# Kernel optimization log

Hardware: AMD Instinct MI355X
Metric: run time of the kernel (lower is better)

## Reference

```python
import jax, jax.numpy as jnp
import numpy as np

B = 4          # documents per batch
L = 128        # unique candidate entity links
S = 2048       # predicted spans (max over batch)
N = 1 + L + S  # root + links + spans


def setup_inputs() -> dict:
    key = jax.random.key(0)
    k1, k2, k3 = jax.random.split(key, 3)
    # coref/linking edge scores over [root | links | spans] x [root | links | spans]
    scores = jax.random.normal(k1, (B, N, N), dtype=jnp.float32) * 0.1
    eye = jnp.eye(N, dtype=jnp.float32)
    # z mask: all admissible edges -- no self loops, no incoming edges to root
    z_mask = jnp.ones((B, N, N), dtype=jnp.float32) * (1.0 - eye)[None]
    z_mask = z_mask.at[:, :, 0].set(0.0)
    # target mask: sparse subset of z edges + root->all so a spanning
    # arborescence always exists (mirrors the gold cluster / gold link edges)
    tgt = (jax.random.uniform(k2, (B, N, N)) < 0.05).astype(jnp.float32) * z_mask
    tgt = tgt.at[:, 0, 1:].set(1.0)
    # ragged valid lengths per batch element (1 + unique_links_len + n_pred_spans)
    lengths = jnp.array([N, N - 256, N - 512, N - 64], dtype=jnp.int32)
    return {"scores": scores, "target_mask": tgt, "z_mask": z_mask, "lengths": lengths}


def _mtt_log_partition(scores, mask, lengths):
    """Matrix-tree theorem log-partition: logdet of the root-minor of the
    Laplacian of exp(scores) restricted to edges in `mask` and to the first
    `lengths[b]` nodes of each batch element."""
    n = scores.shape[-1]
    valid = (jnp.arange(n)[None, :] < lengths[:, None]).astype(scores.dtype)  # [B,N]
    w = jnp.exp(scores) * mask * valid[:, :, None] * valid[:, None, :]        # [B,N,N]
    colsum = jnp.sum(w, axis=-2)                                              # incoming weight per node
    lap = colsum[:, :, None] * jnp.eye(n, dtype=scores.dtype)[None] - w       # L = D_in - W
    minor = lap[:, 1:, 1:]                                                    # drop root row/col
    # pad the diagonal of invalid (past-length) nodes with 1 so they
    # contribute logdet 0 instead of making the minor singular
    pad = 1.0 - valid[:, 1:]
    minor = minor + pad[:, :, None] * jnp.eye(n - 1, dtype=scores.dtype)[None]
    _, logdet = jnp.linalg.slogdet(minor)
    return logdet


def reference(scores, target_mask, z_mask, lengths):
    log_z = _mtt_log_partition(scores, z_mask, lengths)        # log partition over all arborescences
    log_t = _mtt_log_partition(scores, target_mask, lengths)   # log weight of gold arborescences
    return jnp.mean(log_z - log_t)                             # MTT negative log-likelihood
```

## Files before the change

### kernel.cpp

```cpp
#include <hip/hip_runtime.h>
#include <math.h>

#define NFULL 2177
#define NN    2176
#define NB    64
#define NMAT  8
#define NBATCH 4
#define TP    65
#define LTP   132
#define UTP   188
#define QL    (16 * LTP)
#define QU    (16 * UTP)
#define QBUF  (QL + QU)
#define SSZ2  (2 * QBUF)


__global__ void init_cs_kernel(float* __restrict__ cs) {
  int i = blockIdx.x * blockDim.x + threadIdx.x;
  if (i < NMAT * NN) cs[i] = 0.f;
}

__global__ __launch_bounds__(256) void build_fused(const float* __restrict__ scores,
                                                   const float* __restrict__ zm,
                                                   const float* __restrict__ tm,
                                                   const int* __restrict__ lengths,
                                                   float* __restrict__ cs,
                                                   float* __restrict__ M) {
  int c = blockIdx.x * 256 + threadIdx.x;
  if (c >= NN) return;
  int b = blockIdx.z;
  int len = lengths[b];
  int j = c + 1;
  bool jv = (j < len);
  int r0 = blockIdx.y * 64;
  size_t sbase = (size_t)b * NFULL * NFULL + j;
  float az = 0.f, at = 0.f;
  if (blockIdx.y == 0 && jv) {
    float e = __expf(scores[sbase]);
    az += e * zm[sbase];
    at += e * tm[sbase];
  }
  size_t mz = (size_t)b * NN * NN + (size_t)r0 * NN + c;
  size_t mt = (size_t)(NBATCH + b) * NN * NN + (size_t)r0 * NN + c;
  for (int rr = 0; rr < 64; ++rr) {
    int i = r0 + rr + 1;
    float vz = 0.f, vt = 0.f;
    if (jv && i < len) {
      size_t off = sbase + (size_t)i * NFULL;
      float e = __expf(scores[off]);
      vz = e * zm[off];
      vt = e * tm[off];
      az += vz;
      at += vt;
    }
    M[mz] = -vz;
    M[mt] = -vt;
    mz += NN;
    mt += NN;
  }
  if (az != 0.f) atomicAdd(&cs[b * NN + c], az);
  if (at != 0.f) atomicAdd(&cs[(NBATCH + b) * NN + c], at);
}

__global__ void diag_fix(const int* __restrict__ lengths,
                         const float* __restrict__ cs,
                         float* __restrict__ M) {
  int idx = blockIdx.x * 256 + threadIdx.x;
  if (idx >= NMAT * NN) return;
  int mm = idx / NN, c = idx - mm * NN;
  int len = lengths[mm & 3];
  float pad = (c + 1 < len) ? 0.f : 1.f;
  M[(size_t)mm * NN * NN + (size_t)c * NN + c] = cs[idx] + pad;
}


__device__ __forceinline__ void factor64(float* T, int tid) {
  int c = tid & 63, g = tid >> 6;
  for (int j = 0; j < 63; ++j) {
    float inv = 1.0f / T[j * TP + j];
    int rs = j + 1 + ((g - j - 1) & 3);
    if (c == j) {
      for (int r = rs; r < 64; r += 4) T[r * TP + j] *= inv;
    }
    __syncthreads();
    if (c > j) {
      float ujc = T[j * TP + c];
      for (int r = rs; r < 64; r += 4) T[r * TP + c] -= T[r * TP + j] * ujc;
    }
    __syncthreads();
  }
}

__device__ void invert64(const float* T, float* X,
                         float* __restrict__ invUg,
                         float* __restrict__ invLg, int tid) {
  if (tid < 64) {
    int o = (tid >> 5) * 32, jj = tid & 31, j = o + jj;
    X[(o + jj) * TP + j] = 1.0f / T[(o + jj) * TP + (o + jj)];
    for (int i = jj - 1; i >= 0; --i) {
      float s = 0.f;
      for (int t = i + 1; t <= jj; ++t)
        s += T[(o + i) * TP + (o + t)] * X[(o + t) * TP + j];
      X[(o + i) * TP + j] = -s / T[(o + i) * TP + (o + i)];
    }
  }
  __syncthreads();
  for (int e = tid; e < 1024; e += 256) {
    int i = e >> 5, j = e & 31;
    float s = 0.f;
    for (int t = 0; t <= j; ++t)
      s += T[i * TP + 32 + t] * X[(32 + t) * TP + 32 + j];
    X[(32 + i) * TP + j] = s;
  }
  __syncthreads();
  for (int e = tid; e < 1024; e += 256) {
    int i = e >> 5, j = e & 31;
    float s = 0.f;
    for (int t = i; t < 32; ++t)
      s += X[i * TP + t] * X[(32 + t) * TP + j];
    X[i * TP + 32 + j] = -s;
  }
  __syncthreads();
  for (int e = tid; e < 4096; e += 256) {
    int i = e >> 6, j = e & 63;
    float v = 0.f;
    if (i < 32 && j >= 32) v = X[i * TP + j];
    else if ((i >> 5) == (j >> 5) && i <= j) v = X[i * TP + j];
    invUg[e] = v;
  }
  __syncthreads();
  if (tid < 64) {
    int o = (tid >> 5) * 32, jj = tid & 31, j = o + jj;
    X[(o + jj) * TP + j] = 1.0f;
    for (int i = jj + 1; i < 32; ++i) {
      float s = 0.f;
      for (int t = jj; t < i; ++t)
        s += T[(o + i) * TP + (o + t)] * X[(o + t) * TP + j];
      X[(o + i) * TP + j] = -s;
    }
  }
  __syncthreads();
  for (int e = tid; e < 1024; e += 256) {
    int i = e >> 5, j = e & 31;
    float s = 0.f;
    for (int t = j; t < 32; ++t)
      s += T[(32 + i) * TP + t] * X[t * TP + j];
    X[i * TP + 32 + j] = s;
  }
  __syncthreads();
  for (int e = tid; e < 1024; e += 256) {
    int i = e >> 5, j = e & 31;
    float s = 0.f;
    for (int t = 0; t <= i; ++t)
      s += X[(32 + i) * TP + 32 + t] * X[t * TP + 32 + j];
    X[(32 + i) * TP + j] = -s;
  }
  __syncthreads();
  for (int e = tid; e < 4096; e += 256) {
    int i = e >> 6, j = e & 63;
    float v = 0.f;
    if (i >= 32 && j < 32) v = X[i * TP + j];
    else if ((i >> 5) == (j >> 5)) v = (i > j) ? X[i * TP + j] : (i == j ? 1.f : 0.f);
    invLg[e] = v;
  }
}

__global__ __launch_bounds__(256) void factor0(float* __restrict__ Mb,
                                               float* __restrict__ invUb,
                                               float* __restrict__ invLb) {
  __shared__ float T[64 * TP];
  __shared__ float X[64 * TP];
  int m = blockIdx.x, tid = threadIdx.x;
  float* A = Mb + (size_t)m * NN * NN;
  for (int idx = tid; idx < 4096; idx += 256)
    T[(idx >> 6) * TP + (idx & 63)] = A[(size_t)(idx >> 6) * NN + (idx & 63)];
  __syncthreads();
  factor64(T, tid);
  for (int idx = tid; idx < 4096; idx += 256)
    A[(size_t)(idx >> 6) * NN + (idx & 63)] = T[(idx >> 6) * TP + (idx & 63)];
  invert64(T, X, invUb + (size_t)m * 4096, invLb + (size_t)m * 4096, tid);
}

__global__ __launch_bounds__(256) void panel_gemm(float* __restrict__ Mb,
                                                  const float* __restrict__ invUb,
                                                  const float* __restrict__ invLb,
                                                  int k0) {
  __shared__ float Aa[64][68];
  __shared__ float Bb[64][68];
  int m = blockIdx.y, role = blockIdx.z, tid = threadIdx.x;
  float* A = Mb + (size_t)m * NN * NN;
  int obase = k0 + 64 + blockIdx.x * 64;
  if (role == 0) {
    const float* invU = invUb + (size_t)m * 4096;
    for (int idx = tid; idx < 4096; idx += 256) {
      int r = idx >> 6, k = idx & 63;
      Aa[k][r] = A[(size_t)(obase + r) * NN + (k0 + k)];
    }
    for (int idx = tid; idx < 4096; idx += 256)
      Bb[idx >> 6][idx & 63] = invU[idx];
  } else {
    const float* invL = invLb + (size_t)m * 4096;
    for (int idx = tid; idx < 4096; idx += 256) {
      int r = idx >> 6, k = idx & 63;
      Aa[k][r] = invL[(r << 6) + k];
    }
    for (int idx = tid; idx < 4096; idx += 256) {
      int k = idx >> 6, c = idx & 63;
      Bb[k][c] = A[(size_t)(k0 + k) * NN + (obase + c)];
    }
  }
  __syncthreads();
  int c0 = (tid & 15) << 2;
  int r0 = (tid >> 4) << 2;
  float acc[4][4];
#pragma unroll
  for (int i = 0; i < 4; ++i)
#pragma unroll
    for (int jj = 0; jj < 4; ++jj) acc[i][jj] = 0.f;
#pragma unroll 8
  for (int k = 0; k < 64; ++k) {
    float4 a  = *(const float4*)&Aa[k][r0];
    float4 bv = *(const float4*)&Bb[k][c0];
    acc[0][0] += a.x * bv.x; acc[0][1] += a.x * bv.y; acc[0][2] += a.x * bv.z; acc[0][3] += a.x * bv.w;
    acc[1][0] += a.y * bv.x; acc[1][1] += a.y * bv.y; acc[1][2] += a.y * bv.z; acc[1][3] += a.y * bv.w;
    acc[2][0] += a.z * bv.x; acc[2][1] += a.z * bv.y; acc[2][2] += a.z * bv.z; acc[2][3] += a.z * bv.w;
    acc[3][0] += a.w * bv.x; acc[3][1] += a.w * bv.y; acc[3][2] += a.w * bv.z; acc[3][3] += a.w * bv.w;
  }
  if (role == 0) {
#pragma unroll
    for (int i = 0; i < 4; ++i) {
      float4 v = make_float4(acc[i][0], acc[i][1], acc[i][2], acc[i][3]);
      *(float4*)&A[(size_t)(obase + r0 + i) * NN + (k0 + c0)] = v;
    }
  } else {
#pragma unroll
    for (int i = 0; i < 4; ++i) {
      float4 v = make_float4(acc[i][0], acc[i][1], acc[i][2], acc[i][3]);
      *(float4*)&A[(size_t)(k0 + r0 + i) * NN + (obase + c0)] = v;
    }
  }
}


__device__ __forceinline__ void load_quarter_regs(const float* __restrict__ A,
                                                  int rbase, int cbase, int rows, int cols,
                                                  int kb, float* lr, float* ur, int tid) {
#pragma unroll
  for (int s = 0; s < 8; ++s) {
    int idx = tid + s * 256;
    int k = idx & 15, r = idx >> 4;
    int gr = rbase + (r < rows ? r : 0);
    lr[s] = A[(size_t)gr * NN + kb + k];
  }
#pragma unroll
  for (int s = 0; s < 8; ++s) {
    int idx = tid + s * 256;
    int c = idx & 127, k = idx >> 7;
    int gc = cbase + (c < cols ? c : 0);
    ur[s] = A[(size_t)(kb + k) * NN + gc];
  }
}

__device__ __forceinline__ void write_quarter_lds(float* __restrict__ S,
                                                  const float* lr, const float* ur, int tid) {
#pragma unroll
  for (int s = 0; s < 8; ++s) {
    int idx = tid + s * 256;
    int k = idx & 15, r = idx >> 4;
    S[k * LTP + r] = lr[s];
  }
#pragma unroll
  for (int s = 0; s < 8; ++s) {
    int idx = tid + s * 256;
    int c = idx & 127, k = idx >> 7;
    S[QL + k * UTP + c + 4 * (c >> 3)] = ur[s];
  }
}

__global__ __launch_bounds__(256, 2) void trail_gemm(float* __restrict__ Mb,
                                                     float* __restrict__ invUb,
                                                     float* __restrict__ invLb,
                                                     int k0, int do_inv) {
  __shared__ float S[SSZ2];
  int m = blockIdx.x;
  int txt = blockIdx.y, tyt = blockIdx.z;
  float* A = Mb + (size_t)m * NN * NN;
  int base = k0 + NB;
  int rem  = NN - base;
  int rbase = base + tyt * 128, cbase = base + txt * 128;
  int rows = rem - tyt * 128; if (rows > 128) rows = 128;
  int cols = rem - txt * 128; if (cols > 128) cols = 128;
  int tid = threadIdx.x;
  int tx = tid & 15, ty = tid >> 4;
  int rr = ty * 8, cc = tx * 8;
  int ccs = 12 * tx;
  float acc[8][8];
#pragma unroll
  for (int i = 0; i < 8; ++i)
#pragma unroll
    for (int j = 0; j < 8; ++j) acc[i][j] = 0.f;

  float lr[8], ur[8];
  load_quarter_regs(A, rbase, cbase, rows, cols, k0, lr, ur, tid);
  write_quarter_lds(S, lr, ur, tid);
  __syncthreads();

#pragma unroll
  for (int q = 0; q < 4; ++q) {
    if (q < 3)
      load_quarter_regs(A, rbase, cbase, rows, cols, k0 + (q + 1) * 16, lr, ur, tid);
    const float* Sc = S + (q & 1) * QBUF;
#pragma unroll
    for (int k = 0; k < 16; ++k) {
      const float* lp = &Sc[k * LTP + rr];
      const float* up = &Sc[QL + k * UTP + ccs];
      float4 a0 = *(const float4*)lp;
      float4 a1 = *(const float4*)(lp + 4);
      float4 b0 = *(const float4*)up;
      float4 b1 = *(const float4*)(up + 4);
      acc[0][0] += a0.x * b0.x; acc[0][1] += a0.x * b0.y; acc[0][2] += a0.x * b0.z; acc[0][3] += a0.x * b0.w;
      acc[0][4] += a0.x * b1.x; acc[0][5] += a0.x * b1.y; acc[0][6] += a0.x * b1.z; acc[0][7] += a0.x * b1.w;
      acc[1][0] += a0.y * b0.x; acc[1][1] += a0.y * b0.y; acc[1][2] += a0.y * b0.z; acc[1][3] += a0.y * b0.w;
      acc[1][4] += a0.y * b1.x; acc[1][5] += a0.y * b1.y; acc[1][6] += a0.y * b1.z; acc[1][7] += a0.y * b1.w;
      acc[2][0] += a0.z * b0.x; acc[2][1] += a0.z * b0.y; acc[2][2] += a0.z * b0.z; acc[2][3] += a0.z * b0.w;
      acc[2][4] += a0.z * b1.x; acc[2][5] += a0.z * b1.y; acc[2][6] += a0.z * b1.z; acc[2][7] += a0.z * b1.w;
      acc[3][0] += a0.w * b0.x; acc[3][1] += a0.w * b0.y; acc[3][2] += a0.w * b0.z; acc[3][3] += a0.w * b0.w;
      acc[3][4] += a0.w * b1.x; acc[3][5] += a0.w * b1.y; acc[3][6] += a0.w * b1.z; acc[3][7] += a0.w * b1.w;
      acc[4][0] += a1.x * b0.x; acc[4][1] += a1.x * b0.y; acc[4][2] += a1.x * b0.z; acc[4][3] += a1.x * b0.w;
      acc[4][4] += a1.x * b1.x; acc[4][5] += a1.x * b1.y; acc[4][6] += a1.x * b1.z; acc[4][7] += a1.x * b1.w;
      acc[5][0] += a1.y * b0.x; acc[5][1] += a1.y * b0.y; acc[5][2] += a1.y * b0.z; acc[5][3] += a1.y * b0.w;
      acc[5][4] += a1.y * b1.x; acc[5][5] += a1.y * b1.y; acc[5][6] += a1.y * b1.z; acc[5][7] += a1.y * b1.w;
      acc[6][0] += a1.z * b0.x; acc[6][1] += a1.z * b0.y; acc[6][2] += a1.z * b0.z; acc[6][3] += a1.z * b0.w;
      acc[6][4] += a1.z * b1.x; acc[6][5] += a1.z * b1.y; acc[6][6] += a1.z * b1.z; acc[6][7] += a1.z * b1.w;
      acc[7][0] += a1.w * b0.x; acc[7][1] += a1.w * b0.y; acc[7][2] += a1.w * b0.z; acc[7][3] += a1.w * b0.w;
      acc[7][4] += a1.w * b1.x; acc[7][5] += a1.w * b1.y; acc[7][6] += a1.w * b1.z; acc[7][7] += a1.w * b1.w;
    }
    __syncthreads();
    if (q < 3) {
      write_quarter_lds(S + ((q + 1) & 1) * QBUF, lr, ur, tid);
      __syncthreads();
    }
  }

  bool special = (txt == 0 && tyt == 0);
  if (!special) {
    if (cc < cols) {
#pragma unroll
      for (int i = 0; i < 8; ++i) {
        int r = rr + i;
        if (r < rows) {
          float4* p = (float4*)&A[(size_t)(rbase + r) * NN + cbase + cc];
          float4 v0 = p[0], v1 = p[1];
          v0.x -= acc[i][0]; v0.y -= acc[i][1]; v0.z -= acc[i][2]; v0.w -= acc[i][3];
          v1.x -= acc[i][4]; v1.y -= acc[i][5]; v1.z -= acc[i][6]; v1.w -= acc[i][7];
          p[0] = v0; p[1] = v1;
        }
      }
    }
    return;
  }
  float* T = S;
  float* X = S + 4224;
  if (cc < cols) {
#pragma unroll
    for (int i = 0; i < 8; ++i) {
      int r = rr + i;
      if (r < rows) {
        float4* p = (float4*)&A[(size_t)(rbase + r) * NN + cbase + cc];
        float4 v0 = p[0], v1 = p[1];
        v0.x -= acc[i][0]; v0.y -= acc[i][1]; v0.z -= acc[i][2]; v0.w -= acc[i][3];
        v1.x -= acc[i][4]; v1.y -= acc[i][5]; v1.z -= acc[i][6]; v1.w -= acc[i][7];
        if (r < 64 && cc < 64) {
          float* t = &T[r * TP + cc];
          t[0] = v0.x; t[1] = v0.y; t[2] = v0.z; t[3] = v0.w;
          t[4] = v1.x; t[5] = v1.y; t[6] = v1.z; t[7] = v1.w;
        } else {
          p[0] = v0; p[1] = v1;
        }
      }
    }
  }
  __syncthreads();
  factor64(T, tid);
  for (int idx = tid; idx < 4096; idx += 256) {
    int r = idx >> 6, c = idx & 63;
    A[(size_t)(base + r) * NN + base + c] = T[r * TP + c];
  }
  if (do_inv)
    invert64(T, X, invUb + (size_t)m * 4096, invLb + (size_t)m * 4096, tid);
}


__global__ void logdet_kernel(const float* __restrict__ Mb, double* __restrict__ dlog) {
  int m = blockIdx.x;
  const float* A = Mb + (size_t)m * NN * NN;
  double s = 0.0;
  for (int i = threadIdx.x; i < NN; i += 256)
    s += (double)logf(fabsf(A[(size_t)i * NN + i]));
  __shared__ double red[256];
  red[threadIdx.x] = s;
  __syncthreads();
  for (int k = 128; k > 0; k >>= 1) {
    if (threadIdx.x < k) red[threadIdx.x] += red[threadIdx.x + k];
    __syncthreads();
  }
  if (threadIdx.x == 0) dlog[m] = red[0];
}

__global__ void final_kernel(const double* __restrict__ dlog, float* __restrict__ out) {
  if (threadIdx.x == 0) {
    double acc = 0.0;
    for (int b = 0; b < NBATCH; ++b) acc += dlog[b] - dlog[NBATCH + b];
    out[0] = (float)(acc * 0.25);
  }
}


extern "C" void kernel_launch(void* const* d_in, const int* in_sizes, int n_in,
                              void* d_out, int out_size, void* d_ws, size_t ws_size,
                              hipStream_t stream) {
  const float* scores  = (const float*)d_in[0];
  const float* tm      = (const float*)d_in[1];
  const float* zm      = (const float*)d_in[2];
  const int*   lengths = (const int*)d_in[3];
  float* out = (float*)d_out;

  float* M  = (float*)d_ws;
  float* cs = M + (size_t)NMAT * NN * NN;
  double* dlog = (double*)(cs + (size_t)NMAT * NN);
  float* invU = (float*)(dlog + NMAT);
  float* invL = invU + (size_t)NMAT * 4096;

  init_cs_kernel<<<(NMAT * NN + 255) / 256, 256, 0, stream>>>(cs);
  build_fused<<<dim3((NN + 255) / 256, NN / 64, NBATCH), 256, 0, stream>>>(
      scores, zm, tm, lengths, cs, M);
  diag_fix<<<(NMAT * NN + 255) / 256, 256, 0, stream>>>(lengths, cs, M);
  factor0<<<NMAT, 256, 0, stream>>>(M, invU, invL);

  for (int k0 = 0; k0 + NB < NN; k0 += NB) {
    int rem = NN - k0 - NB;
    panel_gemm<<<dim3(rem / 64, NMAT, 2), 256, 0, stream>>>(M, invU, invL, k0);
    int nt = (rem + 127) / 128;
    trail_gemm<<<dim3(NMAT, nt, nt), 256, 0, stream>>>(
        M, invU, invL, k0, rem > 64 ? 1 : 0);
  }

  logdet_kernel<<<NMAT, 256, 0, stream>>>(M, dlog);
  final_kernel<<<1, 64, 0, stream>>>(dlog, out);
}
```

Before: 4.872 ms.

## Fuse LU pipeline into one persistent cooperative kernel with per-matrix ragged bounds

Replaces the per-step panel/trailing kernel launches (about 68 iterations of two launches each) and the setup kernels with a single cooperative persistent kernel that uses grid-wide syncs between phases. Work per step is also trimmed per matrix to the valid length rounded up to 64, so padded identity rows and columns of shorter documents are no longer factored. This removes launch overhead and wasted tiles. In exchange it adds grid.sync costs, runtime job-index decoding, and relies on the occupancy query to size the grid correctly.

```diff
diff --git a/kernel.cpp b/kernel.cpp
--- a/kernel.cpp
+++ b/kernel.cpp
@@ -1,5 +1,8 @@
 #include <hip/hip_runtime.h>
+#include <hip/hip_cooperative_groups.h>
 #include <math.h>
+
+namespace cg = cooperative_groups;
 
 #define NFULL 2177
 #define NN    2176
@@ -15,65 +18,6 @@
 #define SSZ2  (2 * QBUF)
 
 
-__global__ void init_cs_kernel(float* __restrict__ cs) {
-  int i = blockIdx.x * blockDim.x + threadIdx.x;
-  if (i < NMAT * NN) cs[i] = 0.f;
-}
-
-__global__ __launch_bounds__(256) void build_fused(const float* __restrict__ scores,
-                                                   const float* __restrict__ zm,
-                                                   const float* __restrict__ tm,
-                                                   const int* __restrict__ lengths,
-                                                   float* __restrict__ cs,
-                                                   float* __restrict__ M) {
-  int c = blockIdx.x * 256 + threadIdx.x;
-  if (c >= NN) return;
-  int b = blockIdx.z;
-  int len = lengths[b];
-  int j = c + 1;
-  bool jv = (j < len);
-  int r0 = blockIdx.y * 64;
-  size_t sbase = (size_t)b * NFULL * NFULL + j;
-  float az = 0.f, at = 0.f;
-  if (blockIdx.y == 0 && jv) {
-    float e = __expf(scores[sbase]);
-    az += e * zm[sbase];
-    at += e * tm[sbase];
-  }
-  size_t mz = (size_t)b * NN * NN + (size_t)r0 * NN + c;
-  size_t mt = (size_t)(NBATCH + b) * NN * NN + (size_t)r0 * NN + c;
-  for (int rr = 0; rr < 64; ++rr) {
-    int i = r0 + rr + 1;
-    float vz = 0.f, vt = 0.f;
-    if (jv && i < len) {
-      size_t off = sbase + (size_t)i * NFULL;
-      float e = __expf(scores[off]);
-      vz = e * zm[off];
-      vt = e * tm[off];
-      az += vz;
-      at += vt;
-    }
-    M[mz] = -vz;
-    M[mt] = -vt;
-    mz += NN;
-    mt += NN;
-  }
-  if (az != 0.f) atomicAdd(&cs[b * NN + c], az);
-  if (at != 0.f) atomicAdd(&cs[(NBATCH + b) * NN + c], at);
-}
-
-__global__ void diag_fix(const int* __restrict__ lengths,
-                         const float* __restrict__ cs,
-                         float* __restrict__ M) {
-  int idx = blockIdx.x * 256 + threadIdx.x;
-  if (idx >= NMAT * NN) return;
-  int mm = idx / NN, c = idx - mm * NN;
-  int len = lengths[mm & 3];
-  float pad = (c + 1 < len) ? 0.f : 1.f;
-  M[(size_t)mm * NN * NN + (size_t)c * NN + c] = cs[idx] + pad;
-}
-
-
 __device__ __forceinline__ void factor64(float* T, int tid) {
   int c = tid & 63, g = tid >> 6;
   for (int j = 0; j < 63; ++j) {
@@ -165,48 +109,30 @@
   }
 }
 
-__global__ __launch_bounds__(256) void factor0(float* __restrict__ Mb,
-                                               float* __restrict__ invUb,
-                                               float* __restrict__ invLb) {
-  __shared__ float T[64 * TP];
-  __shared__ float X[64 * TP];
-  int m = blockIdx.x, tid = threadIdx.x;
+__device__ void panel_job(float* __restrict__ Mb, const float* __restrict__ invUb,
+                          const float* __restrict__ invLb, int k0,
+                          int m, int role, int px, int tid, float* S) {
+  float* Aa = S;
+  float* Bb = S + 64 * 68;
   float* A = Mb + (size_t)m * NN * NN;
-  for (int idx = tid; idx < 4096; idx += 256)
-    T[(idx >> 6) * TP + (idx & 63)] = A[(size_t)(idx >> 6) * NN + (idx & 63)];
-  __syncthreads();
-  factor64(T, tid);
-  for (int idx = tid; idx < 4096; idx += 256)
-    A[(size_t)(idx >> 6) * NN + (idx & 63)] = T[(idx >> 6) * TP + (idx & 63)];
-  invert64(T, X, invUb + (size_t)m * 4096, invLb + (size_t)m * 4096, tid);
-}
-
-__global__ __launch_bounds__(256) void panel_gemm(float* __restrict__ Mb,
-                                                  const float* __restrict__ invUb,
-                                                  const float* __restrict__ invLb,
-                                                  int k0) {
-  __shared__ float Aa[64][68];
-  __shared__ float Bb[64][68];
-  int m = blockIdx.y, role = blockIdx.z, tid = threadIdx.x;
-  float* A = Mb + (size_t)m * NN * NN;
-  int obase = k0 + 64 + blockIdx.x * 64;
+  int obase = k0 + 64 + px * 64;
   if (role == 0) {
-    const float* invU = invUb + (size_t)m * 4096;
+    const float* iU = invUb + (size_t)m * 4096;
     for (int idx = tid; idx < 4096; idx += 256) {
       int r = idx >> 6, k = idx & 63;
-      Aa[k][r] = A[(size_t)(obase + r) * NN + (k0 + k)];
+      Aa[k * 68 + r] = A[(size_t)(obase + r) * NN + (k0 + k)];
     }
     for (int idx = tid; idx < 4096; idx += 256)
-      Bb[idx >> 6][idx & 63] = invU[idx];
+      Bb[(idx >> 6) * 68 + (idx & 63)] = iU[idx];
   } else {
-    const float* invL = invLb + (size_t)m * 4096;
+    const float* iL = invLb + (size_t)m * 4096;
     for (int idx = tid; idx < 4096; idx += 256) {
       int r = idx >> 6, k = idx & 63;
-      Aa[k][r] = invL[(r << 6) + k];
+      Aa[k * 68 + r] = iL[(r << 6) + k];
     }
     for (int idx = tid; idx < 4096; idx += 256) {
       int k = idx >> 6, c = idx & 63;
-      Bb[k][c] = A[(size_t)(k0 + k) * NN + (obase + c)];
+      Bb[k * 68 + c] = A[(size_t)(k0 + k) * NN + (obase + c)];
     }
   }
   __syncthreads();
@@ -219,8 +145,8 @@
     for (int jj = 0; jj < 4; ++jj) acc[i][jj] = 0.f;
 #pragma unroll 8
   for (int k = 0; k < 64; ++k) {
-    float4 a  = *(const float4*)&Aa[k][r0];
-    float4 bv = *(const float4*)&Bb[k][c0];
+    float4 a  = *(const float4*)&Aa[k * 68 + r0];
+    float4 bv = *(const float4*)&Bb[k * 68 + c0];
     acc[0][0] += a.x * bv.x; acc[0][1] += a.x * bv.y; acc[0][2] += a.x * bv.z; acc[0][3] += a.x * bv.w;
     acc[1][0] += a.y * bv.x; acc[1][1] += a.y * bv.y; acc[1][2] += a.y * bv.z; acc[1][3] += a.y * bv.w;
     acc[2][0] += a.z * bv.x; acc[2][1] += a.z * bv.y; acc[2][2] += a.z * bv.z; acc[2][3] += a.z * bv.w;
@@ -277,20 +203,14 @@
   }
 }
 
-__global__ __launch_bounds__(256, 2) void trail_gemm(float* __restrict__ Mb,
-                                                     float* __restrict__ invUb,
-                                                     float* __restrict__ invLb,
-                                                     int k0, int do_inv) {
-  __shared__ float S[SSZ2];
-  int m = blockIdx.x;
-  int txt = blockIdx.y, tyt = blockIdx.z;
+__device__ void trail_job(float* __restrict__ Mb, float* __restrict__ invUb,
+                          float* __restrict__ invLb, int k0, int remm,
+                          int m, int tyt, int txt, int do_inv, int tid, float* S) {
   float* A = Mb + (size_t)m * NN * NN;
   int base = k0 + NB;
-  int rem  = NN - base;
   int rbase = base + tyt * 128, cbase = base + txt * 128;
-  int rows = rem - tyt * 128; if (rows > 128) rows = 128;
-  int cols = rem - txt * 128; if (cols > 128) cols = 128;
-  int tid = threadIdx.x;
+  int rows = remm - tyt * 128; if (rows > 128) rows = 128;
+  int cols = remm - txt * 128; if (cols > 128) cols = 128;
   int tx = tid & 15, ty = tid >> 4;
   int rr = ty * 8, cc = tx * 8;
   int ccs = 12 * tx;
@@ -391,6 +311,160 @@
 }
 
 
+__global__ __launch_bounds__(256, 3) void lu_coop(const float* __restrict__ scores,
+                                                  const float* __restrict__ zm,
+                                                  const float* __restrict__ tm,
+                                                  const int* __restrict__ lengths,
+                                                  float* __restrict__ M,
+                                                  float* __restrict__ cs,
+                                                  float* __restrict__ invU,
+                                                  float* __restrict__ invL) {
+  __shared__ float S[SSZ2];
+  cg::grid_group grid = cg::this_grid();
+  const int tid = threadIdx.x;
+  const int bid = blockIdx.x;
+  const int G = gridDim.x;
+
+  int nmr[NMAT];
+#pragma unroll
+  for (int mm = 0; mm < NMAT; ++mm) {
+    int nm = lengths[mm & 3] - 1;
+    nm = (nm + 63) & ~63;
+    if (nm < 64) nm = 64;
+    if (nm > NN) nm = NN;
+    nmr[mm] = nm;
+  }
+
+  for (int i = bid * 256 + tid; i < NMAT * NN; i += G * 256) cs[i] = 0.f;
+  grid.sync();
+
+  for (int job = bid; job < 9 * 34 * NBATCH; job += G) {
+    int b = job / (9 * 34);
+    int rj = job - b * (9 * 34);
+    int ry = rj / 9, cx = rj - ry * 9;
+    int c = cx * 256 + tid;
+    if (c < NN) {
+      int len = lengths[b];
+      int j = c + 1;
+      bool jv = (j < len);
+      int r0 = ry * 64;
+      size_t sbase = (size_t)b * NFULL * NFULL + j;
+      float az = 0.f, at = 0.f;
+      if (ry == 0 && jv) {
+        float e = __expf(scores[sbase]);
+        az += e * zm[sbase];
+        at += e * tm[sbase];
+      }
+      size_t mz = (size_t)b * NN * NN + (size_t)r0 * NN + c;
+      size_t mt = (size_t)(NBATCH + b) * NN * NN + (size_t)r0 * NN + c;
+      for (int rrr = 0; rrr < 64; ++rrr) {
+        int i = r0 + rrr + 1;
+        float vz = 0.f, vt = 0.f;
+        if (jv && i < len) {
+          size_t off = sbase + (size_t)i * NFULL;
+          float e = __expf(scores[off]);
+          vz = e * zm[off];
+          vt = e * tm[off];
+          az += vz;
+          at += vt;
+        }
+        M[mz] = -vz;
+        M[mt] = -vt;
+        mz += NN;
+        mt += NN;
+      }
+      if (az != 0.f) atomicAdd(&cs[b * NN + c], az);
+      if (at != 0.f) atomicAdd(&cs[(NBATCH + b) * NN + c], at);
+    }
+  }
+  grid.sync();
+
+  for (int i = bid * 256 + tid; i < NMAT * NN; i += G * 256) {
+    int mm = i / NN, c = i - mm * NN;
+    int len = lengths[mm & 3];
+    float pad = (c + 1 < len) ? 0.f : 1.f;
+    M[(size_t)mm * NN * NN + (size_t)c * NN + c] = cs[i] + pad;
+  }
+  grid.sync();
+
+  if (bid < NMAT) {
+    float* A = M + (size_t)bid * NN * NN;
+    for (int idx = tid; idx < 4096; idx += 256)
+      S[(idx >> 6) * TP + (idx & 63)] = A[(size_t)(idx >> 6) * NN + (idx & 63)];
+    __syncthreads();
+    factor64(S, tid);
+    for (int idx = tid; idx < 4096; idx += 256)
+      A[(size_t)(idx >> 6) * NN + (idx & 63)] = S[(idx >> 6) * TP + (idx & 63)];
+    invert64(S, S + 4224, invU + (size_t)bid * 4096, invL + (size_t)bid * 4096, tid);
+  }
+  grid.sync();
+
+  for (int k0 = 0; k0 + NB < NN; k0 += NB) {
+    int totA = 0;
+#pragma unroll
+    for (int mm = 0; mm < NMAT; ++mm) {
+      int remm = nmr[mm] - k0 - NB;
+      if (remm > 0) totA += 2 * (remm >> 6);
+    }
+    for (int job = bid; job < totA; job += G) {
+      int m = 0, local = 0, bbase = 0;
+#pragma unroll
+      for (int mm = 0; mm < NMAT; ++mm) {
+        int remm = nmr[mm] - k0 - NB;
+        int w = remm > 0 ? 2 * (remm >> 6) : 0;
+        if (job >= bbase && job < bbase + w) { m = mm; local = job - bbase; }
+        bbase += w;
+      }
+      int npt = (nmr[m] - k0 - NB) >> 6;
+      int role = (local >= npt) ? 1 : 0;
+      int px = role ? local - npt : local;
+      __syncthreads();
+      panel_job(M, invU, invL, k0, m, role, px, tid, S);
+    }
+    grid.sync();
+    int totS = 0, totR = 0;
+#pragma unroll
+    for (int mm = 0; mm < NMAT; ++mm) {
+      int remm = nmr[mm] - k0 - NB;
+      if (remm > 0) {
+        int n2 = (remm + 127) >> 7;
+        totS += 1;
+        totR += n2 * n2 - 1;
+      }
+    }
+    int totB = totS + totR;
+    for (int job = bid; job < totB; job += G) {
+      int m = 0, ty = 0, tx = 0;
+      if (job < totS) {
+        int cnt = 0;
+#pragma unroll
+        for (int mm = 0; mm < NMAT; ++mm) {
+          int remm = nmr[mm] - k0 - NB;
+          if (remm > 0) { if (cnt == job) m = mm; ++cnt; }
+        }
+      } else {
+        int jr = job - totS, bbase = 0, tloc = 0;
+#pragma unroll
+        for (int mm = 0; mm < NMAT; ++mm) {
+          int remm = nmr[mm] - k0 - NB;
+          int n2 = remm > 0 ? (remm + 127) >> 7 : 0;
+          int w = n2 > 0 ? n2 * n2 - 1 : 0;
+          if (jr >= bbase && jr < bbase + w) { m = mm; tloc = jr - bbase + 1; }
+          bbase += w;
+        }
+        int n2m = (nmr[m] - k0 - NB + 127) >> 7;
+        ty = tloc / n2m;
+        tx = tloc - ty * n2m;
+      }
+      int remm = nmr[m] - k0 - NB;
+      __syncthreads();
+      trail_job(M, invU, invL, k0, remm, m, ty, tx, (remm > 64) ? 1 : 0, tid, S);
+    }
+    grid.sync();
+  }
+}
+
+
 __global__ void logdet_kernel(const float* __restrict__ Mb, double* __restrict__ dlog) {
   int m = blockIdx.x;
   const float* A = Mb + (size_t)m * NN * NN;
@@ -431,19 +505,28 @@
   float* invU = (float*)(dlog + NMAT);
   float* invL = invU + (size_t)NMAT * 4096;
 
-  init_cs_kernel<<<(NMAT * NN + 255) / 256, 256, 0, stream>>>(cs);
-  build_fused<<<dim3((NN + 255) / 256, NN / 64, NBATCH), 256, 0, stream>>>(
-      scores, zm, tm, lengths, cs, M);
-  diag_fix<<<(NMAT * NN + 255) / 256, 256, 0, stream>>>(lengths, cs, M);
-  factor0<<<NMAT, 256, 0, stream>>>(M, invU, invL);
-
-  for (int k0 = 0; k0 + NB < NN; k0 += NB) {
-    int rem = NN - k0 - NB;
-    panel_gemm<<<dim3(rem / 64, NMAT, 2), 256, 0, stream>>>(M, invU, invL, k0);
-    int nt = (rem + 127) / 128;
-    trail_gemm<<<dim3(NMAT, nt, nt), 256, 0, stream>>>(
-        M, invU, invL, k0, rem > 64 ? 1 : 0);
-  }
+  static int s_grid = 0;
+  if (s_grid == 0) {
+    int nb = 0;
+    if (hipOccupancyMaxActiveBlocksPerMultiprocessor(&nb, (const void*)lu_coop, 256, 0) != hipSuccess || nb <= 0)
+      nb = 3;
+    hipDeviceProp_t prop;
+    int dev = 0;
+    hipGetDevice(&dev);
+    int cus = 256;
+    if (hipGetDeviceProperties(&prop, dev) == hipSuccess && prop.multiProcessorCount > 0)
+      cus = prop.multiProcessorCount;
+    s_grid = nb * cus;
+    if (s_grid < 64) s_grid = 64;
+  }
+
+  const float* s_ = scores; const float* z_ = zm; const float* t_ = tm;
+  const int* l_ = lengths;
+  float* M_ = M; float* cs_ = cs; float* iU_ = invU; float* iL_ = invL;
+  void* kargs[] = {(void*)&s_, (void*)&z_, (void*)&t_, (void*)&l_,
+                   (void*)&M_, (void*)&cs_, (void*)&iU_, (void*)&iL_};
+  hipLaunchCooperativeKernel((const void*)lu_coop, dim3(s_grid), dim3(256),
+                             kargs, 0, stream);
 
   logdet_kernel<<<NMAT, 256, 0, stream>>>(M, dlog);
   final_kernel<<<1, 64, 0, stream>>>(dlog, out);
```

Result: slower. 9.987 ms (+105.0%).

## Fuse panel and trailing LU updates into a flag-synchronized persistent step kernel

Applied to the files above, without the earlier changes.

Each LU step's panel GEMM and trailing update now run in a single lu_step launch instead of two. Blocks pull jobs from an atomic work queue, and trailing tiles spin on per-panel-chunk flags rather than waiting on a kernel boundary. This lets trailing work start while other panel chunks are still finishing and halves the per-step launch count. The job counts are also sized per matrix from the valid length, so the padded identity region past each document's length is skipped. The cost is spin-wait synchronization through global atomics, which relies on panel jobs being dequeued before the tiles that depend on them, plus extra index-decoding work per job.

```diff
diff --git a/kernel.cpp b/kernel.cpp
--- a/kernel.cpp
+++ b/kernel.cpp
@@ -13,65 +13,8 @@
 #define QU    (16 * UTP)
 #define QBUF  (QL + QU)
 #define SSZ2  (2 * QBUF)
-
-
-__global__ void init_cs_kernel(float* __restrict__ cs) {
-  int i = blockIdx.x * blockDim.x + threadIdx.x;
-  if (i < NMAT * NN) cs[i] = 0.f;
-}
-
-__global__ __launch_bounds__(256) void build_fused(const float* __restrict__ scores,
-                                                   const float* __restrict__ zm,
-                                                   const float* __restrict__ tm,
-                                                   const int* __restrict__ lengths,
-                                                   float* __restrict__ cs,
-                                                   float* __restrict__ M) {
-  int c = blockIdx.x * 256 + threadIdx.x;
-  if (c >= NN) return;
-  int b = blockIdx.z;
-  int len = lengths[b];
-  int j = c + 1;
-  bool jv = (j < len);
-  int r0 = blockIdx.y * 64;
-  size_t sbase = (size_t)b * NFULL * NFULL + j;
-  float az = 0.f, at = 0.f;
-  if (blockIdx.y == 0 && jv) {
-    float e = __expf(scores[sbase]);
-    az += e * zm[sbase];
-    at += e * tm[sbase];
-  }
-  size_t mz = (size_t)b * NN * NN + (size_t)r0 * NN + c;
-  size_t mt = (size_t)(NBATCH + b) * NN * NN + (size_t)r0 * NN + c;
-  for (int rr = 0; rr < 64; ++rr) {
-    int i = r0 + rr + 1;
-    float vz = 0.f, vt = 0.f;
-    if (jv && i < len) {
-      size_t off = sbase + (size_t)i * NFULL;
-      float e = __expf(scores[off]);
-      vz = e * zm[off];
-      vt = e * tm[off];
-      az += vz;
-      at += vt;
-    }
-    M[mz] = -vz;
-    M[mt] = -vt;
-    mz += NN;
-    mt += NN;
-  }
-  if (az != 0.f) atomicAdd(&cs[b * NN + c], az);
-  if (at != 0.f) atomicAdd(&cs[(NBATCH + b) * NN + c], at);
-}
-
-__global__ void diag_fix(const int* __restrict__ lengths,
-                         const float* __restrict__ cs,
-                         float* __restrict__ M) {
-  int idx = blockIdx.x * 256 + threadIdx.x;
-  if (idx >= NMAT * NN) return;
-  int mm = idx / NN, c = idx - mm * NN;
-  int len = lengths[mm & 3];
-  float pad = (c + 1 < len) ? 0.f : 1.f;
-  M[(size_t)mm * NN * NN + (size_t)c * NN + c] = cs[idx] + pad;
-}
+#define NCH   34
+#define NIT   34
 
 
 __device__ __forceinline__ void factor64(float* T, int tid) {
@@ -165,48 +108,30 @@
   }
 }
 
-__global__ __launch_bounds__(256) void factor0(float* __restrict__ Mb,
-                                               float* __restrict__ invUb,
-                                               float* __restrict__ invLb) {
-  __shared__ float T[64 * TP];
-  __shared__ float X[64 * TP];
-  int m = blockIdx.x, tid = threadIdx.x;
+__device__ void panel_job(float* __restrict__ Mb, const float* __restrict__ invUb,
+                          const float* __restrict__ invLb, int k0,
+                          int m, int role, int px, int tid, float* S) {
+  float* Aa = S;
+  float* Bb = S + 64 * 68;
   float* A = Mb + (size_t)m * NN * NN;
-  for (int idx = tid; idx < 4096; idx += 256)
-    T[(idx >> 6) * TP + (idx & 63)] = A[(size_t)(idx >> 6) * NN + (idx & 63)];
-  __syncthreads();
-  factor64(T, tid);
-  for (int idx = tid; idx < 4096; idx += 256)
-    A[(size_t)(idx >> 6) * NN + (idx & 63)] = T[(idx >> 6) * TP + (idx & 63)];
-  invert64(T, X, invUb + (size_t)m * 4096, invLb + (size_t)m * 4096, tid);
-}
-
-__global__ __launch_bounds__(256) void panel_gemm(float* __restrict__ Mb,
-                                                  const float* __restrict__ invUb,
-                                                  const float* __restrict__ invLb,
-                                                  int k0) {
-  __shared__ float Aa[64][68];
-  __shared__ float Bb[64][68];
-  int m = blockIdx.y, role = blockIdx.z, tid = threadIdx.x;
-  float* A = Mb + (size_t)m * NN * NN;
-  int obase = k0 + 64 + blockIdx.x * 64;
+  int obase = k0 + 64 + px * 64;
   if (role == 0) {
-    const float* invU = invUb + (size_t)m * 4096;
+    const float* iU = invUb + (size_t)m * 4096;
     for (int idx = tid; idx < 4096; idx += 256) {
       int r = idx >> 6, k = idx & 63;
-      Aa[k][r] = A[(size_t)(obase + r) * NN + (k0 + k)];
+      Aa[k * 68 + r] = A[(size_t)(obase + r) * NN + (k0 + k)];
     }
     for (int idx = tid; idx < 4096; idx += 256)
-      Bb[idx >> 6][idx & 63] = invU[idx];
+      Bb[(idx >> 6) * 68 + (idx & 63)] = iU[idx];
   } else {
-    const float* invL = invLb + (size_t)m * 4096;
+    const float* iL = invLb + (size_t)m * 4096;
     for (int idx = tid; idx < 4096; idx += 256) {
       int r = idx >> 6, k = idx & 63;
-      Aa[k][r] = invL[(r << 6) + k];
+      Aa[k * 68 + r] = iL[(r << 6) + k];
     }
     for (int idx = tid; idx < 4096; idx += 256) {
       int k = idx >> 6, c = idx & 63;
-      Bb[k][c] = A[(size_t)(k0 + k) * NN + (obase + c)];
+      Bb[k * 68 + c] = A[(size_t)(k0 + k) * NN + (obase + c)];
     }
   }
   __syncthreads();
@@ -219,8 +144,8 @@
     for (int jj = 0; jj < 4; ++jj) acc[i][jj] = 0.f;
 #pragma unroll 8
   for (int k = 0; k < 64; ++k) {
-    float4 a  = *(const float4*)&Aa[k][r0];
-    float4 bv = *(const float4*)&Bb[k][c0];
+    float4 a  = *(const float4*)&Aa[k * 68 + r0];
+    float4 bv = *(const float4*)&Bb[k * 68 + c0];
     acc[0][0] += a.x * bv.x; acc[0][1] += a.x * bv.y; acc[0][2] += a.x * bv.z; acc[0][3] += a.x * bv.w;
     acc[1][0] += a.y * bv.x; acc[1][1] += a.y * bv.y; acc[1][2] += a.y * bv.z; acc[1][3] += a.y * bv.w;
     acc[2][0] += a.z * bv.x; acc[2][1] += a.z * bv.y; acc[2][2] += a.z * bv.z; acc[2][3] += a.z * bv.w;
@@ -277,20 +202,14 @@
   }
 }
 
-__global__ __launch_bounds__(256, 2) void trail_gemm(float* __restrict__ Mb,
-                                                     float* __restrict__ invUb,
-                                                     float* __restrict__ invLb,
-                                                     int k0, int do_inv) {
-  __shared__ float S[SSZ2];
-  int m = blockIdx.x;
-  int txt = blockIdx.y, tyt = blockIdx.z;
+__device__ void trail_job(float* __restrict__ Mb, float* __restrict__ invUb,
+                          float* __restrict__ invLb, int k0, int remm,
+                          int m, int tyt, int txt, int do_inv, int tid, float* S) {
   float* A = Mb + (size_t)m * NN * NN;
   int base = k0 + NB;
-  int rem  = NN - base;
   int rbase = base + tyt * 128, cbase = base + txt * 128;
-  int rows = rem - tyt * 128; if (rows > 128) rows = 128;
-  int cols = rem - txt * 128; if (cols > 128) cols = 128;
-  int tid = threadIdx.x;
+  int rows = remm - tyt * 128; if (rows > 128) rows = 128;
+  int cols = remm - txt * 128; if (cols > 128) cols = 128;
   int tx = tid & 15, ty = tid >> 4;
   int rr = ty * 8, cc = tx * 8;
   int ccs = 12 * tx;
@@ -391,6 +310,190 @@
 }
 
 
+__global__ void init_all(float* __restrict__ cs, int* __restrict__ qctr,
+                         int* __restrict__ Lf, int* __restrict__ Uf) {
+  int i = blockIdx.x * blockDim.x + threadIdx.x;
+  if (i < NMAT * NN) cs[i] = 0.f;
+  if (i < NIT) qctr[i] = 0;
+  if (i < NMAT * NCH) { Lf[i] = 0; Uf[i] = 0; }
+}
+
+__global__ __launch_bounds__(256) void build_fused(const float* __restrict__ scores,
+                                                   const float* __restrict__ zm,
+                                                   const float* __restrict__ tm,
+                                                   const int* __restrict__ lengths,
+                                                   float* __restrict__ cs,
+                                                   float* __restrict__ M) {
+  int c = blockIdx.x * 256 + threadIdx.x;
+  if (c >= NN) return;
+  int b = blockIdx.z;
+  int len = lengths[b];
+  int j = c + 1;
+  bool jv = (j < len);
+  int r0 = blockIdx.y * 64;
+  size_t sbase = (size_t)b * NFULL * NFULL + j;
+  float az = 0.f, at = 0.f;
+  if (blockIdx.y == 0 && jv) {
+    float e = __expf(scores[sbase]);
+    az += e * zm[sbase];
+    at += e * tm[sbase];
+  }
+  size_t mz = (size_t)b * NN * NN + (size_t)r0 * NN + c;
+  size_t mt = (size_t)(NBATCH + b) * NN * NN + (size_t)r0 * NN + c;
+  for (int rr = 0; rr < 64; ++rr) {
+    int i = r0 + rr + 1;
+    float vz = 0.f, vt = 0.f;
+    if (jv && i < len) {
+      size_t off = sbase + (size_t)i * NFULL;
+      float e = __expf(scores[off]);
+      vz = e * zm[off];
+      vt = e * tm[off];
+      az += vz;
+      at += vt;
+    }
+    M[mz] = -vz;
+    M[mt] = -vt;
+    mz += NN;
+    mt += NN;
+  }
+  if (az != 0.f) atomicAdd(&cs[b * NN + c], az);
+  if (at != 0.f) atomicAdd(&cs[(NBATCH + b) * NN + c], at);
+}
+
+__global__ void diag_fix(const int* __restrict__ lengths,
+                         const float* __restrict__ cs,
+                         float* __restrict__ M) {
+  int idx = blockIdx.x * 256 + threadIdx.x;
+  if (idx >= NMAT * NN) return;
+  int mm = idx / NN, c = idx - mm * NN;
+  int len = lengths[mm & 3];
+  float pad = (c + 1 < len) ? 0.f : 1.f;
+  M[(size_t)mm * NN * NN + (size_t)c * NN + c] = cs[idx] + pad;
+}
+
+__global__ __launch_bounds__(256) void factor0(float* __restrict__ Mb,
+                                               float* __restrict__ invUb,
+                                               float* __restrict__ invLb) {
+  __shared__ float T[64 * TP];
+  __shared__ float X[64 * TP];
+  int m = blockIdx.x, tid = threadIdx.x;
+  float* A = Mb + (size_t)m * NN * NN;
+  for (int idx = tid; idx < 4096; idx += 256)
+    T[(idx >> 6) * TP + (idx & 63)] = A[(size_t)(idx >> 6) * NN + (idx & 63)];
+  __syncthreads();
+  factor64(T, tid);
+  for (int idx = tid; idx < 4096; idx += 256)
+    A[(size_t)(idx >> 6) * NN + (idx & 63)] = T[(idx >> 6) * TP + (idx & 63)];
+  invert64(T, X, invUb + (size_t)m * 4096, invLb + (size_t)m * 4096, tid);
+}
+
+
+__device__ __forceinline__ void wait_flags(int* fl, int nl, int* fu, int nu,
+                                           int kseq, int tid) {
+  if (tid == 0) {
+    for (int i = 0; i < nl; ++i)
+      while (atomicAdd(fl + i, 0) < kseq) __builtin_amdgcn_s_sleep(2);
+    for (int i = 0; i < nu; ++i)
+      while (atomicAdd(fu + i, 0) < kseq) __builtin_amdgcn_s_sleep(2);
+    __threadfence();
+  }
+  __syncthreads();
+}
+
+__global__ __launch_bounds__(256, 2) void lu_step(float* __restrict__ M,
+                                                  float* __restrict__ invU,
+                                                  float* __restrict__ invL,
+                                                  const int* __restrict__ lengths,
+                                                  int* __restrict__ qctr,
+                                                  int* __restrict__ Lf,
+                                                  int* __restrict__ Uf,
+                                                  int k0, int kidx) {
+  __shared__ float S[SSZ2];
+  __shared__ int Sjob;
+  const int tid = threadIdx.x;
+  const int kseq = kidx + 1;
+
+  int nmr[NMAT];
+#pragma unroll
+  for (int mm = 0; mm < NMAT; ++mm) {
+    int nm = lengths[mm & 3] - 1;
+    nm = (nm + 63) & ~63;
+    if (nm < 64) nm = 64;
+    if (nm > NN) nm = NN;
+    nmr[mm] = nm;
+  }
+
+  int totP = 0, totS = 0, totT = 0;
+#pragma unroll
+  for (int mm = 0; mm < NMAT; ++mm) {
+    int rm = nmr[mm] - k0 - NB;
+    if (rm > 0) {
+      totP += 2 * (rm >> 6);
+      totS += 1;
+      int n2 = (rm + 127) >> 7;
+      totT += n2 * n2 - 1;
+    }
+  }
+  int totB = totP + totS + totT;
+
+  for (;;) {
+    __syncthreads();
+    if (tid == 0) Sjob = atomicAdd(&qctr[kidx], 1);
+    __syncthreads();
+    int job = Sjob;
+    if (job >= totB) return;
+
+    if (job < totP) {
+      int m = 0, local = 0, bbase = 0;
+#pragma unroll
+      for (int mm = 0; mm < NMAT; ++mm) {
+        int rm = nmr[mm] - k0 - NB;
+        int w = rm > 0 ? 2 * (rm >> 6) : 0;
+        if (job >= bbase && job < bbase + w) { m = mm; local = job - bbase; }
+        bbase += w;
+      }
+      int npt = (nmr[m] - k0 - NB) >> 6;
+      int role = (local >= npt) ? 1 : 0;
+      int px = role ? local - npt : local;
+      panel_job(M, invU, invL, k0, m, role, px, tid, S);
+      __syncthreads();
+      if (tid == 0) {
+        __threadfence();
+        atomicExch(((role == 0) ? Lf : Uf) + m * NCH + px, kseq);
+      }
+    } else {
+      int jr = job - totP;
+      int m = 0, ty = 0, tx = 0, remm = 64;
+      if (jr < totS) {
+        int cnt = 0;
+#pragma unroll
+        for (int mm = 0; mm < NMAT; ++mm) {
+          int rm = nmr[mm] - k0 - NB;
+          if (rm > 0) { if (cnt == jr) { m = mm; remm = rm; } ++cnt; }
+        }
+      } else {
+        int jt = jr - totS, bbase = 0, tloc = 0;
+#pragma unroll
+        for (int mm = 0; mm < NMAT; ++mm) {
+          int rm = nmr[mm] - k0 - NB;
+          int n2 = rm > 0 ? (rm + 127) >> 7 : 0;
+          int w = n2 > 0 ? n2 * n2 - 1 : 0;
+          if (jt >= bbase && jt < bbase + w) { m = mm; remm = rm; tloc = jt - bbase + 1; }
+          bbase += w;
+        }
+        int n2m = (remm + 127) >> 7;
+        ty = tloc / n2m;
+        tx = tloc - ty * n2m;
+      }
+      int nch = remm >> 6;
+      wait_flags(Lf + m * NCH + 2 * ty, (2 * ty + 1 < nch) ? 2 : 1,
+                 Uf + m * NCH + 2 * tx, (2 * tx + 1 < nch) ? 2 : 1, kseq, tid);
+      trail_job(M, invU, invL, k0, remm, m, ty, tx, (remm > 64) ? 1 : 0, tid, S);
+    }
+  }
+}
+
+
 __global__ void logdet_kernel(const float* __restrict__ Mb, double* __restrict__ dlog) {
   int m = blockIdx.x;
   const float* A = Mb + (size_t)m * NN * NN;
@@ -430,19 +533,23 @@
   double* dlog = (double*)(cs + (size_t)NMAT * NN);
   float* invU = (float*)(dlog + NMAT);
   float* invL = invU + (size_t)NMAT * 4096;
-
-  init_cs_kernel<<<(NMAT * NN + 255) / 256, 256, 0, stream>>>(cs);
+  int* qctr = (int*)(invL + (size_t)NMAT * 4096);
+  int* Lf = qctr + NIT;
+  int* Uf = Lf + NMAT * NCH;
+
+  init_all<<<(NMAT * NN + 255) / 256, 256, 0, stream>>>(cs, qctr, Lf, Uf);
   build_fused<<<dim3((NN + 255) / 256, NN / 64, NBATCH), 256, 0, stream>>>(
       scores, zm, tm, lengths, cs, M);
   diag_fix<<<(NMAT * NN + 255) / 256, 256, 0, stream>>>(lengths, cs, M);
   factor0<<<NMAT, 256, 0, stream>>>(M, invU, invL);
 
-  for (int k0 = 0; k0 + NB < NN; k0 += NB) {
-    int rem = NN - k0 - NB;
-    panel_gemm<<<dim3(rem / 64, NMAT, 2), 256, 0, stream>>>(M, invU, invL, k0);
-    int nt = (rem + 127) / 128;
-    trail_gemm<<<dim3(NMAT, nt, nt), 256, 0, stream>>>(
-        M, invU, invL, k0, rem > 64 ? 1 : 0);
+  int kidx = 0;
+  for (int k0 = 0; k0 + NB < NN; k0 += NB, ++kidx) {
+    int remX = NN - k0 - NB;
+    int n2 = (remX + 127) / 128;
+    int tot = NMAT * 2 * (remX / 64) + NMAT * n2 * n2;
+    int G = tot < 2048 ? tot : 2048;
+    lu_step<<<G, 256, 0, stream>>>(M, invU, invL, lengths, qctr, Lf, Uf, k0, kidx);
   }
 
   logdet_kernel<<<NMAT, 256, 0, stream>>>(M, dlog);
```

Result: slower. 7.321 ms (+50.3%).
